# Performance work log

Measured on AMD Instinct MI355X. Metric: run time of the kernel, lower is better.

## Reference

```python
import jax, jax.numpy as jnp
import numpy as np

MAX_DISP = 48


def setup_inputs() -> dict:
    key = jax.random.key(0)
    k1, k2 = jax.random.split(key)
    n, c, h, w = 2, 32, 128, 256
    l_fmap = jax.random.normal(k1, (n, c, h, w), dtype=jnp.float32)
    r_fmap = jax.random.normal(k2, (n, c, h, w), dtype=jnp.float32)
    return {"l_fmap": l_fmap, "r_fmap": r_fmap}


def reference(l_fmap, r_fmap):
    # Cost volume: out[n,c,d,h,x] = l[n,c,h,x] - r[n,c,h,x-d] for x >= d, else 1.0
    n, c, h, w = l_fmap.shape
    d = jnp.arange(MAX_DISP)                      # [D]
    shift = jnp.arange(w)[None, :] - d[:, None]   # [D, W] source column in r
    valid = shift >= 0                            # [D, W]
    r_g = r_fmap[:, :, :, jnp.clip(shift, 0)]     # [n, c, h, D, W] gather of shifted right fmap
    one = jnp.asarray(1.0, l_fmap.dtype)
    cost = jnp.where(valid[None, None, None], l_fmap[:, :, :, None, :] - r_g, one)
    return jnp.transpose(cost, (0, 1, 3, 2, 4))   # [n, c, D, h, W]
```

## Files before the change

### kernel.cpp

```cpp
#include <hip/hip_runtime.h>

#define MAX_DISP 48


constexpr int W = 256;
constexpr int H = 128;

__global__ __launch_bounds__(256) void cost_volume_kernel(
    const float* __restrict__ l,
    const float* __restrict__ r,
    float* __restrict__ out)
{
    const int row = blockIdx.x;
    const int h   = row % H;
    const int nc  = row / H;

    __shared__ float rs[W];

    const int t = threadIdx.x;
    const float* __restrict__ lrow = l + (size_t)row * W;
    const float* __restrict__ rrow = r + (size_t)row * W;

    rs[t] = rrow[t];
    __syncthreads();

    const int lane_d = t >> 6;
    const int xq     = (t & 63) << 2;

    const float4 lv = *reinterpret_cast<const float4*>(lrow + xq);

    float* __restrict__ obase = out + (size_t)nc * MAX_DISP * H * W + (size_t)h * W;

    #pragma unroll
    for (int dpass = 0; dpass < MAX_DISP; dpass += 4) {
        const int d = dpass + lane_d;
        const float r0 = rs[max(xq + 0 - d, 0)];
        const float r1 = rs[max(xq + 1 - d, 0)];
        const float r2 = rs[max(xq + 2 - d, 0)];
        const float r3 = rs[max(xq + 3 - d, 0)];
        float4 o;
        o.x = (xq + 0 >= d) ? lv.x - r0 : 1.0f;
        o.y = (xq + 1 >= d) ? lv.y - r1 : 1.0f;
        o.z = (xq + 2 >= d) ? lv.z - r2 : 1.0f;
        o.w = (xq + 3 >= d) ? lv.w - r3 : 1.0f;
        *reinterpret_cast<float4*>(obase + (size_t)d * H * W + xq) = o;
    }
}

extern "C" void kernel_launch(void* const* d_in, const int* in_sizes, int n_in,
                              void* d_out, int out_size, void* d_ws, size_t ws_size,
                              hipStream_t stream)
{
    const float* l = (const float*)d_in[0];
    const float* r = (const float*)d_in[1];
    float* out = (float*)d_out;

    const int nRows = 2 * 32 * H;
    cost_volume_kernel<<<nRows, 256, 0, stream>>>(l, r, out);
}
```

Baseline: 82.19 us.

## Assign one block per (nc, disparity) plane with contiguous output writes

```diff
diff --git a/kernel.cpp b/kernel.cpp
--- a/kernel.cpp
+++ b/kernel.cpp
@@ -3,47 +3,45 @@
 #define MAX_DISP 48
 
 
-constexpr int W = 256;
-constexpr int H = 128;
+constexpr int W  = 256;
+constexpr int H  = 128;
+constexpr int D  = MAX_DISP;
+constexpr int NC = 64;
 
 __global__ __launch_bounds__(256) void cost_volume_kernel(
     const float* __restrict__ l,
     const float* __restrict__ r,
     float* __restrict__ out)
 {
-    const int row = blockIdx.x;
-    const int h   = row % H;
-    const int nc  = row / H;
+    const int b  = blockIdx.x;
+    const int d  = b % D;
+    const int nc = b / D;
 
-    __shared__ float rs[W];
+    const float* __restrict__ lp = l + (size_t)nc * H * W;
+    const float* __restrict__ rp = r + (size_t)nc * H * W;
+    float* __restrict__ op = out + (size_t)b * H * W;
 
     const int t = threadIdx.x;
-    const float* __restrict__ lrow = l + (size_t)row * W;
-    const float* __restrict__ rrow = r + (size_t)row * W;
-
-    rs[t] = rrow[t];
-    __syncthreads();
-
-    const int lane_d = t >> 6;
-    const int xq     = (t & 63) << 2;
-
-    const float4 lv = *reinterpret_cast<const float4*>(lrow + xq);
-
-    float* __restrict__ obase = out + (size_t)nc * MAX_DISP * H * W + (size_t)h * W;
 
     #pragma unroll
-    for (int dpass = 0; dpass < MAX_DISP; dpass += 4) {
-        const int d = dpass + lane_d;
-        const float r0 = rs[max(xq + 0 - d, 0)];
-        const float r1 = rs[max(xq + 1 - d, 0)];
-        const float r2 = rs[max(xq + 2 - d, 0)];
-        const float r3 = rs[max(xq + 3 - d, 0)];
+    for (int k = 0; k < (H * W / 4) / 256; ++k) {
+        const int flat = (t + k * 256) * 4;
+        const int x    = flat & (W - 1);
+
+        const float4 lv = *reinterpret_cast<const float4*>(lp + flat);
+
+        const float r0 = rp[max(flat + 0 - d, 0)];
+        const float r1 = rp[max(flat + 1 - d, 0)];
+        const float r2 = rp[max(flat + 2 - d, 0)];
+        const float r3 = rp[max(flat + 3 - d, 0)];
+
         float4 o;
-        o.x = (xq + 0 >= d) ? lv.x - r0 : 1.0f;
-        o.y = (xq + 1 >= d) ? lv.y - r1 : 1.0f;
-        o.z = (xq + 2 >= d) ? lv.z - r2 : 1.0f;
-        o.w = (xq + 3 >= d) ? lv.w - r3 : 1.0f;
-        *reinterpret_cast<float4*>(obase + (size_t)d * H * W + xq) = o;
+        o.x = (x + 0 >= d) ? lv.x - r0 : 1.0f;
+        o.y = (x + 1 >= d) ? lv.y - r1 : 1.0f;
+        o.z = (x + 2 >= d) ? lv.z - r2 : 1.0f;
+        o.w = (x + 3 >= d) ? lv.w - r3 : 1.0f;
+
+        *reinterpret_cast<float4*>(op + flat) = o;
     }
 }
 
@@ -55,6 +53,5 @@
     const float* r = (const float*)d_in[1];
     float* out = (float*)d_out;
 
-    const int nRows = 2 * 32 * H;
-    cost_volume_kernel<<<nRows, 256, 0, stream>>>(l, r, out);
+    cost_volume_kernel<<<NC * D, 256, 0, stream>>>(l, r, out);
 }
```

Result: slower. 144.9 us (+76.3%).
